# Kernel tuning notes

Hardware: AMD Instinct MI355X
Metric: run time of the kernel (lower is better)

Reference implementation:

```python
import jax, jax.numpy as jnp
import numpy as np

N_HEADS = 16

def setup_inputs() -> dict:
    key = jax.random.key(0)
    ks = jax.random.split(key, 4)
    B, T, C = 4, 2048, 1024
    x = jax.random.normal(ks[0], (B, T, C), dtype=jnp.float32)
    w_qkv = jax.random.normal(ks[1], (C, 3 * C), dtype=jnp.float32) * (1.0 / np.sqrt(C))
    b_qkv = jnp.zeros((3 * C,), dtype=jnp.float32)
    w_proj = jax.random.normal(ks[2], (C, C), dtype=jnp.float32) * (1.0 / np.sqrt(C))
    b_proj = jnp.zeros((C,), dtype=jnp.float32)
    return {"x": x, "w_qkv": w_qkv, "b_qkv": b_qkv, "w_proj": w_proj, "b_proj": b_proj}

def reference(x, w_qkv, b_qkv, w_proj, b_proj):
    B, T, C = x.shape
    H = N_HEADS
    d = C // H
    qkv = x @ w_qkv + b_qkv                       # [B,T,3C]
    q, k, v = jnp.split(qkv, 3, axis=-1)
    # [B,T,C] -> [B,H,T,d]
    q = q.reshape(B, T, H, d).transpose(0, 2, 1, 3)
    k = k.reshape(B, T, H, d).transpose(0, 2, 1, 3)
    v = v.reshape(B, T, H, d).transpose(0, 2, 1, 3)
    scale = 1.0 / np.sqrt(d).astype(np.float32)
    logits = jnp.einsum('bhqd,bhkd->bhqk', q, k) * scale  # [B,H,T,T]
    causal = jnp.tril(jnp.ones((T, T), dtype=bool))
    logits = jnp.where(causal, logits, jnp.finfo(logits.dtype).min)
    attn = jax.nn.softmax(logits, axis=-1)
    out = jnp.einsum('bhqk,bhkd->bhqd', attn, v)          # [B,H,T,d]
    out = out.transpose(0, 2, 1, 3).reshape(B, T, C)
    return out @ w_proj + b_proj
```

## Files before the change

kernel.cpp:

```cpp
#include <hip/hip_runtime.h>
#include <hip/hip_bf16.h>


typedef unsigned short u16;
typedef __bf16 bf16_t;
typedef bf16_t bf16x8 __attribute__((ext_vector_type(8)));
typedef float f32x4 __attribute__((ext_vector_type(4)));
typedef u16 u16x8 __attribute__((ext_vector_type(8)));
typedef const __attribute__((address_space(1))) void* as1cv;
typedef __attribute__((address_space(3))) void* as3v;

#define BB 4
#define TT 2048
#define CC 1024
#define HH 16
#define DD 64

static __device__ __forceinline__ u16 f2bf(float f) {
  union { float f; unsigned int u; } x; x.f = f;
  unsigned int u = x.u;
  u += 0x7fff + ((u >> 16) & 1);
  return (u16)(u >> 16);
}

static __device__ __forceinline__ unsigned int pack2(float lo, float hi) {
  return __builtin_amdgcn_perm(__float_as_uint(hi), __float_as_uint(lo),
                               0x07060302u);
}

__global__ __launch_bounds__(256) void cast_f32_bf16(
    const float* __restrict__ in, u16* __restrict__ out) {
  int i = (blockIdx.x * 256 + threadIdx.x) * 4;
  float4 v = *(const float4*)(in + i);
  ushort4 o;
  o.x = f2bf(v.x); o.y = f2bf(v.y); o.z = f2bf(v.z); o.w = f2bf(v.w);
  *(ushort4*)(out + i) = o;
}

__global__ __launch_bounds__(256) void transpose_cast(
    const float* __restrict__ in, u16* __restrict__ out, int K, int N) {
  __shared__ float tile[32][33];
  int n0 = blockIdx.x * 32, k0 = blockIdx.y * 32;
  int tx = threadIdx.x & 31, ty = threadIdx.x >> 5;
#pragma unroll
  for (int i = 0; i < 32; i += 8)
    tile[ty + i][tx] = in[(size_t)(k0 + ty + i) * N + n0 + tx];
  __syncthreads();
#pragma unroll
  for (int i = 0; i < 32; i += 8)
    out[(size_t)(n0 + ty + i) * K + k0 + tx] = f2bf(tile[tx][ty + i]);
}

__global__ __launch_bounds__(256) void gemm_bt(
    const u16* __restrict__ A, const u16* __restrict__ Bt,
    const float* __restrict__ bias,
    int M, int N, int K, int mode,
    u16* __restrict__ qb, u16* __restrict__ kb, u16* __restrict__ vt,
    float* __restrict__ outf) {
  __shared__ u16 As[128][64];
  __shared__ u16 Bs[128][64];
  const int tid = threadIdx.x;
  const int lane = tid & 63, wave = tid >> 6;
  const int quad = lane >> 4, l16 = lane & 15;
  const int wy = wave >> 1, wx = wave & 1;
  const int m0 = blockIdx.x * 128, n0 = blockIdx.y * 128;
  const int srow = lane >> 3, sblk = (lane & 7) ^ (lane >> 3);
  const int rsw = l16 & 7;

  f32x4 acc[4][4] = {};

  for (int k0 = 0; k0 < K; k0 += 64) {
#pragma unroll
    for (int i = 0; i < 4; i++) {
      int lr = wave * 32 + i * 8;
      int row = lr + srow;
      __builtin_amdgcn_global_load_lds(
          (as1cv)(A + (size_t)(m0 + row) * K + k0 + sblk * 8),
          (as3v)(&As[lr][0]), 16, 0, 0);
      __builtin_amdgcn_global_load_lds(
          (as1cv)(Bt + (size_t)(n0 + row) * K + k0 + sblk * 8),
          (as3v)(&Bs[lr][0]), 16, 0, 0);
    }
    __syncthreads();
#pragma unroll
    for (int ks = 0; ks < 2; ks++) {
      const int pcol = ((ks * 4 + quad) ^ rsw) * 8;
      bf16x8 af[4], bfr[4];
#pragma unroll
      for (int i = 0; i < 4; i++)
        af[i] = *(const bf16x8*)&As[wy * 64 + i * 16 + l16][pcol];
#pragma unroll
      for (int j = 0; j < 4; j++)
        bfr[j] = *(const bf16x8*)&Bs[wx * 64 + j * 16 + l16][pcol];
#pragma unroll
      for (int i = 0; i < 4; i++)
#pragma unroll
        for (int j = 0; j < 4; j++)
          acc[i][j] = __builtin_amdgcn_mfma_f32_16x16x32_bf16(af[i], bfr[j], acc[i][j], 0, 0, 0);
    }
    __syncthreads();
  }

  if (mode == 1) {
#pragma unroll
    for (int i = 0; i < 4; i++)
#pragma unroll
      for (int j = 0; j < 4; j++) {
        int nn = n0 + wx * 64 + j * 16 + l16;
        float bv = bias[nn];
#pragma unroll
        for (int r = 0; r < 4; r++) {
          int mm = m0 + wy * 64 + i * 16 + quad * 4 + r;
          outf[(size_t)mm * N + nn] = acc[i][j][r] + bv;
        }
      }
  } else {
    const int b = m0 >> 11;
    const int tb = (m0 & 2047) + wy * 64 + quad * 4;
    if (n0 < 1024) {
#pragma unroll
      for (int j = 0; j < 4; j++) {
        int nn = n0 + wx * 64 + j * 16 + l16;
        int h = nn >> 6, dd = nn & 63;
        float bv = bias[nn];
        u16* base = qb + ((size_t)(b * HH + h) * TT) * DD + dd;
#pragma unroll
        for (int i = 0; i < 4; i++)
#pragma unroll
          for (int r = 0; r < 4; r++)
            base[(size_t)(tb + i * 16 + r) * DD] =
                f2bf((acc[i][j][r] + bv) * 0.1803368801111f);
      }
    } else if (n0 < 2048) {
#pragma unroll
      for (int j = 0; j < 4; j++) {
        int nn = n0 + wx * 64 + j * 16 + l16;
        int rem = nn & 1023, h = rem >> 6, dd = rem & 63;
        float bv = bias[nn];
        u16* base = kb + ((size_t)(b * HH + h) * TT) * DD + dd;
#pragma unroll
        for (int i = 0; i < 4; i++)
#pragma unroll
          for (int r = 0; r < 4; r++)
            base[(size_t)(tb + i * 16 + r) * DD] = f2bf(acc[i][j][r] + bv);
      }
    } else {
#pragma unroll
      for (int j = 0; j < 4; j++) {
        int nn = n0 + wx * 64 + j * 16 + l16;
        int rem = nn & 1023, h = rem >> 6, dd = rem & 63;
        float bv = bias[nn];
        u16* base = vt + ((size_t)(b * HH + h) * DD + dd) * TT;
#pragma unroll
        for (int i = 0; i < 4; i++)
#pragma unroll
          for (int r = 0; r < 4; r++)
            base[tb + i * 16 + r] = f2bf(acc[i][j][r] + bv);
      }
    }
  }
}

__global__ __launch_bounds__(256, 3) void attn_kernel(
    const u16* __restrict__ q_buf, const u16* __restrict__ k_buf,
    const u16* __restrict__ v_t, u16* __restrict__ attn_out) {
  __shared__ __align__(16) u16 Ks[2][64][64];
  __shared__ __align__(16) u16 Vs[2][64][64];
  __shared__ __align__(16) u16 Pl[4][16][64];
  const int tid = threadIdx.x;
  const int lane = tid & 63, wave = tid >> 6;
  const int quad = lane >> 4, l16 = lane & 15;
  const int bh = blockIdx.x;
  const int b = bh >> 4, h = bh & 15;
  const int tile = 15 - (int)blockIdx.y;
  const int qt0 = tile * 128;
  const int qw = qt0 + wave * 32;
  const u16* Q = q_buf + (size_t)bh * TT * DD;
  const u16* Kp = k_buf + (size_t)bh * TT * DD;
  const u16* Vt = v_t + (size_t)bh * DD * TT;

  const int srow = lane >> 3;
  const int sblk = (lane & 7) ^ srow;
  const int swz = l16 & 7;

  bf16x8 qf[2][2];
#pragma unroll
  for (int f = 0; f < 2; f++)
#pragma unroll
    for (int h2 = 0; h2 < 2; h2++)
      qf[f][h2] = *(const bf16x8*)(Q + (size_t)(qw + f * 16 + l16) * DD + h2 * 32 + quad * 8);

  f32x4 o[2][4] = {};
  float l_p[2] = {0.f, 0.f};

  const int my_end = qw + 32;
  const int kv_stop = qt0 + 128;
  for (int kv0 = 0; kv0 < kv_stop; kv0 += 128) {
#pragma unroll
    for (int hh = 0; hh < 2; hh++)
#pragma unroll
      for (int i = 0; i < 2; i++) {
        int r = wave * 16 + i * 8 + srow;
        __builtin_amdgcn_global_load_lds(
            (as1cv)(Kp + (size_t)(kv0 + hh * 64 + r) * DD + sblk * 8),
            (as3v)(&Ks[hh][wave * 16 + i * 8][0]), 16, 0, 0);
        __builtin_amdgcn_global_load_lds(
            (as1cv)(Vt + (size_t)r * TT + kv0 + hh * 64 + sblk * 8),
            (as3v)(&Vs[hh][wave * 16 + i * 8][0]), 16, 0, 0);
      }
    __syncthreads();

#pragma unroll
    for (int hh = 0; hh < 2; hh++) {
      const int kb0 = kv0 + hh * 64;
      if (kb0 < my_end) {
        const bool edge = (kb0 + 63 > qw);
        f32x4 s[2][4] = {};
#pragma unroll
        for (int kg = 0; kg < 4; kg++) {
          bf16x8 ka = *(const bf16x8*)&Ks[hh][kg * 16 + l16][(quad ^ swz) * 8];
          bf16x8 kb2 = *(const bf16x8*)&Ks[hh][kg * 16 + l16][((4 + quad) ^ swz) * 8];
#pragma unroll
          for (int f = 0; f < 2; f++) {
            s[f][kg] = __builtin_amdgcn_mfma_f32_16x16x32_bf16(ka, qf[f][0], s[f][kg], 0, 0, 0);
            s[f][kg] = __builtin_amdgcn_mfma_f32_16x16x32_bf16(kb2, qf[f][1], s[f][kg], 0, 0, 0);
          }
        }
#pragma unroll
        for (int f = 0; f < 2; f++) {
          const int qi = qw + f * 16 + l16;
#pragma unroll
          for (int kg = 0; kg < 4; kg++) {
            float v0 = s[f][kg][0], v1 = s[f][kg][1], v2 = s[f][kg][2], v3 = s[f][kg][3];
            if (edge) {
              int kvb = kb0 + kg * 16 + quad * 4;
              v0 = (kvb + 0 <= qi) ? v0 : -1e30f;
              v1 = (kvb + 1 <= qi) ? v1 : -1e30f;
              v2 = (kvb + 2 <= qi) ? v2 : -1e30f;
              v3 = (kvb + 3 <= qi) ? v3 : -1e30f;
            }
            float e0 = __builtin_amdgcn_exp2f(v0);
            float e1 = __builtin_amdgcn_exp2f(v1);
            float e2 = __builtin_amdgcn_exp2f(v2);
            float e3 = __builtin_amdgcn_exp2f(v3);
            l_p[f] += (e0 + e1) + (e2 + e3);
            uint2 pk;
            pk.x = pack2(e0, e1);
            pk.y = pack2(e2, e3);
            *(uint2*)&Pl[wave][l16][((kg * 2 + (quad >> 1)) ^ swz) * 8 + (quad & 1) * 4] = pk;
          }
          __threadfence_block();
#pragma unroll
          for (int c = 0; c < 2; c++) {
            bf16x8 pa = *(const bf16x8*)&Pl[wave][l16][((c * 4 + quad) ^ swz) * 8];
#pragma unroll
            for (int g = 0; g < 4; g++) {
              bf16x8 vr = *(const bf16x8*)&Vs[hh][g * 16 + l16][((c * 4 + quad) ^ swz) * 8];
              o[f][g] = __builtin_amdgcn_mfma_f32_16x16x32_bf16(vr, pa, o[f][g], 0, 0, 0);
            }
          }
        }
      }
    }
    __syncthreads();
  }

#pragma unroll
  for (int f = 0; f < 2; f++) {
    float l = l_p[f];
    l += __shfl_xor(l, 16);
    l += __shfl_xor(l, 32);
    float inv_l = 1.0f / l;
    int trow = qw + f * 16 + l16;
#pragma unroll
    for (int g = 0; g < 4; g++) {
      ushort4 st;
      st.x = f2bf(o[f][g][0] * inv_l);
      st.y = f2bf(o[f][g][1] * inv_l);
      st.z = f2bf(o[f][g][2] * inv_l);
      st.w = f2bf(o[f][g][3] * inv_l);
      *(ushort4*)(attn_out + ((size_t)(b * TT + trow)) * CC + h * DD + g * 16 + quad * 4) = st;
    }
  }
}

extern "C" void kernel_launch(void* const* d_in, const int* in_sizes, int n_in,
                              void* d_out, int out_size, void* d_ws, size_t ws_size,
                              hipStream_t stream) {
  const float* x = (const float*)d_in[0];
  const float* w_qkv = (const float*)d_in[1];
  const float* b_qkv = (const float*)d_in[2];
  const float* w_proj = (const float*)d_in[3];
  const float* b_proj = (const float*)d_in[4];
  float* out = (float*)d_out;
  char* ws = (char*)d_ws;

  u16* wqkvT = (u16*)(ws);
  u16* wprojT = (u16*)(ws + 6291456);
  u16* qb = (u16*)(ws + 8388608);
  u16* kb = (u16*)(ws + 25165824);
  u16* vt = (u16*)(ws + 41943040);
  u16* ao = (u16*)(ws + 58720256);
  u16* xb = ao;

  cast_f32_bf16<<<dim3(8192), 256, 0, stream>>>(x, xb);
  transpose_cast<<<dim3(96, 32), 256, 0, stream>>>(w_qkv, wqkvT, 1024, 3072);
  transpose_cast<<<dim3(32, 32), 256, 0, stream>>>(w_proj, wprojT, 1024, 1024);
  gemm_bt<<<dim3(64, 24), 256, 0, stream>>>(xb, wqkvT, b_qkv, 8192, 3072, 1024, 0,
                                            qb, kb, vt, nullptr);
  attn_kernel<<<dim3(64, 16), 256, 0, stream>>>(qb, kb, vt, ao);
  gemm_bt<<<dim3(64, 8), 256, 0, stream>>>(ao, wprojT, b_proj, 8192, 1024, 1024, 1,
                                           nullptr, nullptr, nullptr, out);
}
```

Baseline: 242.7 us.

## Replace QKV GEMM with 256x256-tile double-buffered 8-wave MFMA kernel

Adds a dedicated QKV projection kernel that uses 256x256 output tiles with 512 threads and double-buffered LDS filled by direct global-to-LDS loads. The main loop interleaves LDS fragment reads, prefetch of the next K tiles and MFMA bursts under s_setprio, and blocks are remapped so neighbouring blocks share A and B panels. The aim is more data reuse per tile and load latency hidden behind compute in the largest GEMM. The trade-off is heavy register and LDS use (128 KB), which may limit occupancy, plus a grid of only 384 blocks that can leave some CUs idle in the last wave.

```diff
diff --git a/kernel.cpp b/kernel.cpp
--- a/kernel.cpp
+++ b/kernel.cpp
@@ -49,6 +49,176 @@
 #pragma unroll
   for (int i = 0; i < 32; i += 8)
     out[(size_t)(n0 + ty + i) * K + k0 + tx] = f2bf(tile[tx][ty + i]);
+}
+
+__global__ __launch_bounds__(512, 2) void gemm_qkv256(
+    const u16* __restrict__ A, const u16* __restrict__ Bt,
+    const float* __restrict__ bias,
+    u16* __restrict__ qb, u16* __restrict__ kb, u16* __restrict__ vt) {
+  constexpr int K = 1024;
+  constexpr int NT = 16;
+  __shared__ u16 As[2][256][64];
+  __shared__ u16 Bs[2][256][64];
+  const int tid = threadIdx.x;
+  const int lane = tid & 63, wave = tid >> 6;
+  const int quad = lane >> 4, l16 = lane & 15;
+  const int wr = wave >> 2, wc = wave & 3;
+  const int rsw = l16 & 7;
+  const int srow8 = tid >> 3;
+  const int sblk = (lane & 7) ^ (lane >> 3);
+
+  const int id = blockIdx.x;
+  const int ch = id & 7, w = id >> 3;
+  const int mi = (ch & 3) * 8 + w / 6;
+  const int ni = (ch >> 2) * 6 + w % 6;
+  const int m0 = mi * 256, n0 = ni * 256;
+
+  const u16* Ab = A + (size_t)(m0 + srow8) * K + sblk * 8;
+  const u16* Bb = Bt + (size_t)(n0 + srow8) * K + sblk * 8;
+
+#define SA_(bufd, h, j, kt) __builtin_amdgcn_global_load_lds(              \
+    (as1cv)(Ab + ((h) * 128 + (j) * 64) * K + (kt) * 64),                  \
+    (as3v)(&As[bufd][(h) * 128 + (j) * 64 + wave * 8][0]), 16, 0, 0)
+#define SB_(bufd, h, j, kt) __builtin_amdgcn_global_load_lds(              \
+    (as1cv)(Bb + ((h) * 128 + (j) * 64) * K + (kt) * 64),                  \
+    (as3v)(&Bs[bufd][(h) * 128 + (j) * 64 + wave * 8][0]), 16, 0, 0)
+#define LDA_(mf, ks) (*(const bf16x8*)&As[buf][wr * 128 + (mf) * 16 + l16] \
+                                         [(((ks) * 4 + quad) ^ rsw) * 8])
+#define LDB_(nf, ks) (*(const bf16x8*)&Bs[buf][wc * 64 + (nf) * 16 + l16]  \
+                                         [(((ks) * 4 + quad) ^ rsw) * 8])
+
+  SB_(0, 0, 0, 0); SB_(0, 0, 1, 0); SB_(0, 1, 0, 0); SB_(0, 1, 1, 0);
+  SA_(0, 0, 0, 0); SA_(0, 0, 1, 0); SA_(0, 1, 0, 0); SA_(0, 1, 1, 0);
+  SB_(1, 0, 0, 1); SB_(1, 0, 1, 1); SB_(1, 1, 0, 1); SB_(1, 1, 1, 1);
+  SA_(1, 0, 0, 1); SA_(1, 0, 1, 1);
+  asm volatile("s_waitcnt vmcnt(6)" ::: "memory");
+  __builtin_amdgcn_s_barrier();
+
+  f32x4 acc[8][4] = {};
+
+#pragma unroll 2
+  for (int t = 0; t < NT; ++t) {
+    const int buf = t & 1;
+    bf16x8 bfr[4][2], a01[2][2], a23[2][2], a47[4][2];
+
+#pragma unroll
+    for (int nf = 0; nf < 4; nf++) { bfr[nf][0] = LDB_(nf, 0); bfr[nf][1] = LDB_(nf, 1); }
+#pragma unroll
+    for (int mf = 0; mf < 2; mf++) { a01[mf][0] = LDA_(mf, 0); a01[mf][1] = LDA_(mf, 1); }
+    if (t + 1 < NT) { SA_(buf ^ 1, 1, 0, t + 1); SA_(buf ^ 1, 1, 1, t + 1); }
+    __builtin_amdgcn_s_barrier();
+    asm volatile("s_waitcnt lgkmcnt(0)" ::: "memory");
+    __builtin_amdgcn_s_setprio(1);
+#pragma unroll
+    for (int mf = 0; mf < 2; mf++)
+#pragma unroll
+      for (int nf = 0; nf < 4; nf++) {
+        acc[mf][nf] = __builtin_amdgcn_mfma_f32_16x16x32_bf16(a01[mf][0], bfr[nf][0], acc[mf][nf], 0, 0, 0);
+        acc[mf][nf] = __builtin_amdgcn_mfma_f32_16x16x32_bf16(a01[mf][1], bfr[nf][1], acc[mf][nf], 0, 0, 0);
+      }
+    __builtin_amdgcn_s_setprio(0);
+    __builtin_amdgcn_s_barrier();
+
+#pragma unroll
+    for (int mf = 0; mf < 2; mf++) { a23[mf][0] = LDA_(2 + mf, 0); a23[mf][1] = LDA_(2 + mf, 1); }
+    if (t + 2 < NT) { SB_(buf, 0, 0, t + 2); SB_(buf, 0, 1, t + 2); }
+    __builtin_amdgcn_s_barrier();
+    asm volatile("s_waitcnt lgkmcnt(0)" ::: "memory");
+    __builtin_amdgcn_s_setprio(1);
+#pragma unroll
+    for (int mf = 0; mf < 2; mf++)
+#pragma unroll
+      for (int nf = 0; nf < 4; nf++) {
+        acc[2 + mf][nf] = __builtin_amdgcn_mfma_f32_16x16x32_bf16(a23[mf][0], bfr[nf][0], acc[2 + mf][nf], 0, 0, 0);
+        acc[2 + mf][nf] = __builtin_amdgcn_mfma_f32_16x16x32_bf16(a23[mf][1], bfr[nf][1], acc[2 + mf][nf], 0, 0, 0);
+      }
+    __builtin_amdgcn_s_setprio(0);
+    __builtin_amdgcn_s_barrier();
+
+#pragma unroll
+    for (int mf = 0; mf < 4; mf++) { a47[mf][0] = LDA_(4 + mf, 0); a47[mf][1] = LDA_(4 + mf, 1); }
+    if (t + 2 < NT) { SB_(buf, 1, 0, t + 2); SB_(buf, 1, 1, t + 2); }
+    __builtin_amdgcn_s_barrier();
+    asm volatile("s_waitcnt lgkmcnt(0)" ::: "memory");
+    __builtin_amdgcn_s_setprio(1);
+#pragma unroll
+    for (int mf = 0; mf < 2; mf++)
+#pragma unroll
+      for (int nf = 0; nf < 4; nf++) {
+        acc[4 + mf][nf] = __builtin_amdgcn_mfma_f32_16x16x32_bf16(a47[mf][0], bfr[nf][0], acc[4 + mf][nf], 0, 0, 0);
+        acc[4 + mf][nf] = __builtin_amdgcn_mfma_f32_16x16x32_bf16(a47[mf][1], bfr[nf][1], acc[4 + mf][nf], 0, 0, 0);
+      }
+    __builtin_amdgcn_s_setprio(0);
+    __builtin_amdgcn_s_barrier();
+
+    if (t + 2 < NT) { SA_(buf, 0, 0, t + 2); SA_(buf, 0, 1, t + 2); }
+    __builtin_amdgcn_s_barrier();
+    __builtin_amdgcn_s_setprio(1);
+#pragma unroll
+    for (int mf = 0; mf < 2; mf++)
+#pragma unroll
+      for (int nf = 0; nf < 4; nf++) {
+        acc[6 + mf][nf] = __builtin_amdgcn_mfma_f32_16x16x32_bf16(a47[2 + mf][0], bfr[nf][0], acc[6 + mf][nf], 0, 0, 0);
+        acc[6 + mf][nf] = __builtin_amdgcn_mfma_f32_16x16x32_bf16(a47[2 + mf][1], bfr[nf][1], acc[6 + mf][nf], 0, 0, 0);
+      }
+    __builtin_amdgcn_s_setprio(0);
+    if (t < NT - 2) asm volatile("s_waitcnt vmcnt(6)" ::: "memory");
+    else            asm volatile("s_waitcnt vmcnt(0)" ::: "memory");
+    __builtin_amdgcn_s_barrier();
+  }
+#undef SA_
+#undef SB_
+#undef LDA_
+#undef LDB_
+
+  const int b = m0 >> 11;
+  const int tb = (m0 & 2047) + wr * 128 + quad * 4;
+  const int seg = n0 >> 10;
+  if (seg == 0) {
+#pragma unroll
+    for (int nf = 0; nf < 4; nf++) {
+      int nn = n0 + wc * 64 + nf * 16 + l16;
+      int hh = (nn & 1023) >> 6, dd = nn & 63;
+      float bv = bias[nn];
+      u16* base = qb + ((size_t)(b * HH + hh) * TT) * DD + dd;
+#pragma unroll
+      for (int mf = 0; mf < 8; mf++)
+#pragma unroll
+        for (int r = 0; r < 4; r++)
+          base[(size_t)(tb + mf * 16 + r) * DD] =
+              f2bf((acc[mf][nf][r] + bv) * 0.1803368801111f);
+    }
+  } else if (seg == 1) {
+#pragma unroll
+    for (int nf = 0; nf < 4; nf++) {
+      int nn = n0 + wc * 64 + nf * 16 + l16;
+      int hh = (nn & 1023) >> 6, dd = nn & 63;
+      float bv = bias[nn];
+      u16* base = kb + ((size_t)(b * HH + hh) * TT) * DD + dd;
+#pragma unroll
+      for (int mf = 0; mf < 8; mf++)
+#pragma unroll
+        for (int r = 0; r < 4; r++)
+          base[(size_t)(tb + mf * 16 + r) * DD] = f2bf(acc[mf][nf][r] + bv);
+    }
+  } else {
+#pragma unroll
+    for (int nf = 0; nf < 4; nf++) {
+      int nn = n0 + wc * 64 + nf * 16 + l16;
+      int hh = (nn & 1023) >> 6, dd = nn & 63;
+      float bv = bias[nn];
+      u16* base = vt + ((size_t)(b * HH + hh) * DD + dd) * TT + tb;
+#pragma unroll
+      for (int mf = 0; mf < 8; mf++) {
+        ushort4 st;
+        st.x = f2bf(acc[mf][nf][0] + bv);
+        st.y = f2bf(acc[mf][nf][1] + bv);
+        st.z = f2bf(acc[mf][nf][2] + bv);
+        st.w = f2bf(acc[mf][nf][3] + bv);
+        *(ushort4*)(base + mf * 16) = st;
+      }
+    }
+  }
 }
 
 __global__ __launch_bounds__(256) void gemm_bt(
@@ -306,8 +476,7 @@
   cast_f32_bf16<<<dim3(8192), 256, 0, stream>>>(x, xb);
   transpose_cast<<<dim3(96, 32), 256, 0, stream>>>(w_qkv, wqkvT, 1024, 3072);
   transpose_cast<<<dim3(32, 32), 256, 0, stream>>>(w_proj, wprojT, 1024, 1024);
-  gemm_bt<<<dim3(64, 24), 256, 0, stream>>>(xb, wqkvT, b_qkv, 8192, 3072, 1024, 0,
-                                            qb, kb, vt, nullptr);
+  gemm_qkv256<<<dim3(384), 512, 0, stream>>>(xb, wqkvT, b_qkv, qb, kb, vt);
   attn_kernel<<<dim3(64, 16), 256, 0, stream>>>(qb, kb, vt, ao);
   gemm_bt<<<dim3(64, 8), 256, 0, stream>>>(ao, wprojT, b_proj, 8192, 1024, 1024, 1,
                                            nullptr, nullptr, nullptr, out);
```

After: 247.1 us. No clear change (+1.8%).

## Double-buffer K/V tiles in 64-row chunks and raise MFMA wave priority

Applied to the files above, without the earlier changes.

The attention loop now walks K/V in 64-key chunks over two LDS buffers. It prefetches the next chunk with global_load_lds while computing the current one, replacing the old scheme of loading 128 keys and then computing. That leaves one barrier per chunk instead of a load-barrier-compute-barrier sequence, so global load latency can overlap with MFMA and exp work. It also wraps the QK and PV MFMA sections in s_setprio to favour matrix issue. The risks are that the prefetch relies on the end-of-iteration barrier waiting for the outstanding LDS loads, and that smaller chunks add more loop iterations.

```diff
diff --git a/kernel.cpp b/kernel.cpp
--- a/kernel.cpp
+++ b/kernel.cpp
@@ -194,72 +194,87 @@
   float l_p[2] = {0.f, 0.f};
 
   const int my_end = qw + 32;
-  const int kv_stop = qt0 + 128;
-  for (int kv0 = 0; kv0 < kv_stop; kv0 += 128) {
-#pragma unroll
-    for (int hh = 0; hh < 2; hh++)
+  const int nc = (qt0 + 128) >> 6;
+
+#pragma unroll
+  for (int i = 0; i < 2; i++) {
+    int r = wave * 16 + i * 8 + srow;
+    __builtin_amdgcn_global_load_lds(
+        (as1cv)(Kp + (size_t)r * DD + sblk * 8),
+        (as3v)(&Ks[0][wave * 16 + i * 8][0]), 16, 0, 0);
+    __builtin_amdgcn_global_load_lds(
+        (as1cv)(Vt + (size_t)(wave * 16 + i * 8 + srow) * TT + sblk * 8),
+        (as3v)(&Vs[0][wave * 16 + i * 8][0]), 16, 0, 0);
+  }
+  __syncthreads();
+
+  for (int c = 0; c < nc; ++c) {
+    const int buf = c & 1;
+    if (c + 1 < nc) {
+      const int kvn = (c + 1) << 6;
 #pragma unroll
       for (int i = 0; i < 2; i++) {
         int r = wave * 16 + i * 8 + srow;
         __builtin_amdgcn_global_load_lds(
-            (as1cv)(Kp + (size_t)(kv0 + hh * 64 + r) * DD + sblk * 8),
-            (as3v)(&Ks[hh][wave * 16 + i * 8][0]), 16, 0, 0);
+            (as1cv)(Kp + (size_t)(kvn + r) * DD + sblk * 8),
+            (as3v)(&Ks[buf ^ 1][wave * 16 + i * 8][0]), 16, 0, 0);
         __builtin_amdgcn_global_load_lds(
-            (as1cv)(Vt + (size_t)r * TT + kv0 + hh * 64 + sblk * 8),
-            (as3v)(&Vs[hh][wave * 16 + i * 8][0]), 16, 0, 0);
-      }
-    __syncthreads();
-
-#pragma unroll
-    for (int hh = 0; hh < 2; hh++) {
-      const int kb0 = kv0 + hh * 64;
-      if (kb0 < my_end) {
-        const bool edge = (kb0 + 63 > qw);
-        f32x4 s[2][4] = {};
+            (as1cv)(Vt + (size_t)r * TT + kvn + sblk * 8),
+            (as3v)(&Vs[buf ^ 1][wave * 16 + i * 8][0]), 16, 0, 0);
+      }
+    }
+
+    const int kb0 = c << 6;
+    if (kb0 < my_end) {
+      const bool edge = (kb0 + 63 > qw);
+      f32x4 s[2][4] = {};
+      __builtin_amdgcn_s_setprio(1);
+#pragma unroll
+      for (int kg = 0; kg < 4; kg++) {
+        bf16x8 ka = *(const bf16x8*)&Ks[buf][kg * 16 + l16][(quad ^ swz) * 8];
+        bf16x8 kb2 = *(const bf16x8*)&Ks[buf][kg * 16 + l16][((4 + quad) ^ swz) * 8];
+#pragma unroll
+        for (int f = 0; f < 2; f++) {
+          s[f][kg] = __builtin_amdgcn_mfma_f32_16x16x32_bf16(ka, qf[f][0], s[f][kg], 0, 0, 0);
+          s[f][kg] = __builtin_amdgcn_mfma_f32_16x16x32_bf16(kb2, qf[f][1], s[f][kg], 0, 0, 0);
+        }
+      }
+      __builtin_amdgcn_s_setprio(0);
+#pragma unroll
+      for (int f = 0; f < 2; f++) {
+        const int qi = qw + f * 16 + l16;
 #pragma unroll
         for (int kg = 0; kg < 4; kg++) {
-          bf16x8 ka = *(const bf16x8*)&Ks[hh][kg * 16 + l16][(quad ^ swz) * 8];
-          bf16x8 kb2 = *(const bf16x8*)&Ks[hh][kg * 16 + l16][((4 + quad) ^ swz) * 8];
-#pragma unroll
-          for (int f = 0; f < 2; f++) {
-            s[f][kg] = __builtin_amdgcn_mfma_f32_16x16x32_bf16(ka, qf[f][0], s[f][kg], 0, 0, 0);
-            s[f][kg] = __builtin_amdgcn_mfma_f32_16x16x32_bf16(kb2, qf[f][1], s[f][kg], 0, 0, 0);
+          float v0 = s[f][kg][0], v1 = s[f][kg][1], v2 = s[f][kg][2], v3 = s[f][kg][3];
+          if (edge) {
+            int kvb = kb0 + kg * 16 + quad * 4;
+            v0 = (kvb + 0 <= qi) ? v0 : -1e30f;
+            v1 = (kvb + 1 <= qi) ? v1 : -1e30f;
+            v2 = (kvb + 2 <= qi) ? v2 : -1e30f;
+            v3 = (kvb + 3 <= qi) ? v3 : -1e30f;
+          }
+          float e0 = __builtin_amdgcn_exp2f(v0);
+          float e1 = __builtin_amdgcn_exp2f(v1);
+          float e2 = __builtin_amdgcn_exp2f(v2);
+          float e3 = __builtin_amdgcn_exp2f(v3);
+          l_p[f] += (e0 + e1) + (e2 + e3);
+          uint2 pk;
+          pk.x = pack2(e0, e1);
+          pk.y = pack2(e2, e3);
+          *(uint2*)&Pl[wave][l16][((kg * 2 + (quad >> 1)) ^ swz) * 8 + (quad & 1) * 4] = pk;
+        }
+        __threadfence_block();
+        __builtin_amdgcn_s_setprio(1);
+#pragma unroll
+        for (int cc = 0; cc < 2; cc++) {
+          bf16x8 pa = *(const bf16x8*)&Pl[wave][l16][((cc * 4 + quad) ^ swz) * 8];
+#pragma unroll
+          for (int g = 0; g < 4; g++) {
+            bf16x8 vr = *(const bf16x8*)&Vs[buf][g * 16 + l16][((cc * 4 + quad) ^ swz) * 8];
+            o[f][g] = __builtin_amdgcn_mfma_f32_16x16x32_bf16(vr, pa, o[f][g], 0, 0, 0);
           }
         }
-#pragma unroll
-        for (int f = 0; f < 2; f++) {
-          const int qi = qw + f * 16 + l16;
-#pragma unroll
-          for (int kg = 0; kg < 4; kg++) {
-            float v0 = s[f][kg][0], v1 = s[f][kg][1], v2 = s[f][kg][2], v3 = s[f][kg][3];
-            if (edge) {
-              int kvb = kb0 + kg * 16 + quad * 4;
-              v0 = (kvb + 0 <= qi) ? v0 : -1e30f;
-              v1 = (kvb + 1 <= qi) ? v1 : -1e30f;
-              v2 = (kvb + 2 <= qi) ? v2 : -1e30f;
-              v3 = (kvb + 3 <= qi) ? v3 : -1e30f;
-            }
-            float e0 = __builtin_amdgcn_exp2f(v0);
-            float e1 = __builtin_amdgcn_exp2f(v1);
-            float e2 = __builtin_amdgcn_exp2f(v2);
-            float e3 = __builtin_amdgcn_exp2f(v3);
-            l_p[f] += (e0 + e1) + (e2 + e3);
-            uint2 pk;
-            pk.x = pack2(e0, e1);
-            pk.y = pack2(e2, e3);
-            *(uint2*)&Pl[wave][l16][((kg * 2 + (quad >> 1)) ^ swz) * 8 + (quad & 1) * 4] = pk;
-          }
-          __threadfence_block();
-#pragma unroll
-          for (int c = 0; c < 2; c++) {
-            bf16x8 pa = *(const bf16x8*)&Pl[wave][l16][((c * 4 + quad) ^ swz) * 8];
-#pragma unroll
-            for (int g = 0; g < 4; g++) {
-              bf16x8 vr = *(const bf16x8*)&Vs[hh][g * 16 + l16][((c * 4 + quad) ^ swz) * 8];
-              o[f][g] = __builtin_amdgcn_mfma_f32_16x16x32_bf16(vr, pa, o[f][g], 0, 0, 0);
-            }
-          }
-        }
+        __builtin_amdgcn_s_setprio(0);
       }
     }
     __syncthreads();
```

After: 248.8 us. 2.5% more time.
